# Kernel tuning notes

Measured on AMD Instinct MI355X. Metric: run time of the kernel, lower is better.

## Reference

```python
import jax, jax.numpy as jnp
import numpy as np

B, S, H, SSZ, IN = 1024, 100, 128, 100, 2


def _gru(x, h, Wih, Whh, bih, bhh):
    # PyTorch GRU cell: gates ordered (reset, update, new)
    gx = x @ Wih.T + bih
    gh = h @ Whh.T + bhh
    xr, xz, xn = jnp.split(gx, 3, axis=-1)
    hr, hz, hn = jnp.split(gh, 3, axis=-1)
    r = jax.nn.sigmoid(xr + hr)
    z = jax.nn.sigmoid(xz + hz)
    n = jnp.tanh(xn + r * hn)
    return (1.0 - z) * n + z * h


def _attn(inst_h, rnn_out, W, v):
    # inst_h: [B,S,H], rnn_out: [B,H] -> softmax attention weights [B,S]
    h = jnp.concatenate([inst_h, jnp.broadcast_to(rnn_out[:, None, :], inst_h.shape)], axis=-1)
    s = jax.nn.relu(jnp.einsum('bsk,kh->bsh', h, W)) @ v
    return jax.nn.softmax(s, axis=1)


def setup_inputs() -> dict:
    key = jax.random.key(0)
    k = jax.random.split(key, 32)
    p = lambda i, shape, sc=0.05: sc * jax.random.normal(k[i], shape, jnp.float32)
    instance = jax.random.uniform(k[0], (B, S, IN), jnp.float32)
    # solutions must be per-row permutations of node indices
    solution_1 = jnp.argsort(jax.random.uniform(k[1], (B, S)), axis=1).astype(jnp.int32)
    solution_2 = jnp.argsort(jax.random.uniform(k[2], (B, S)), axis=1).astype(jnp.int32)
    eps = jax.random.normal(k[3], (B, SSZ), jnp.float32)
    return dict(
        instance=instance, solution_1=solution_1, solution_2=solution_2, eps=eps,
        emb_i_W=p(4, (H, IN)), emb_i_b=jnp.zeros(H, jnp.float32),
        emb_r_W=p(5, (H, IN)), emb_r_b=jnp.zeros(H, jnp.float32),
        attn_W=p(6, (2 * H, H)), attn_v=p(7, (H,)),
        gru_Wih=p(8, (3 * H, H)), gru_Whh=p(9, (3 * H, H)),
        gru_bih=jnp.zeros(3 * H, jnp.float32), gru_bhh=jnp.zeros(3 * H, jnp.float32),
        grud_Wih=p(10, (3 * H, 2 * H)), grud_Whh=p(11, (3 * H, H)),
        grud_bih=jnp.zeros(3 * H, jnp.float32), grud_bhh=jnp.zeros(3 * H, jnp.float32),
        enc_fc1_W=p(12, (SSZ, H)), enc_fc1_b=jnp.zeros(SSZ, jnp.float32),
        enc_fc2_W=p(13, (SSZ, H)), enc_fc2_b=jnp.zeros(SSZ, jnp.float32),
        ptr_W=p(14, (2 * H, H)), ptr_v=p(15, (H,)),
        pfc1_W=p(16, (2 * H, 2 * H + SSZ)), pfc1_b=jnp.zeros(2 * H, jnp.float32),
        pfc2_W=p(17, (H, 2 * H)), pfc2_b=jnp.zeros(H, jnp.float32),
    )


def reference(instance, solution_1, solution_2, eps,
              emb_i_W, emb_i_b, emb_r_W, emb_r_b, attn_W, attn_v,
              gru_Wih, gru_Whh, gru_bih, gru_bhh,
              grud_Wih, grud_Whh, grud_bih, grud_bhh,
              enc_fc1_W, enc_fc1_b, enc_fc2_W, enc_fc2_b,
              ptr_W, ptr_v, pfc1_W, pfc1_b, pfc2_W, pfc2_b):
    b_idx = jnp.arange(B)
    inst_h = instance @ emb_i_W.T + emb_i_b  # [B,S,H]
    emb_r = lambda x: x @ emb_r_W.T + emb_r_b
    take = lambda ptr: instance[b_idx, ptr]  # gather node coords [B,IN]

    # ---------------- Encoder ----------------
    def enc_step(carry, ptr):
        h1, h2, ref_h = carry
        h1 = _gru(ref_h, h1, gru_Wih, gru_Whh, gru_bih, gru_bhh)
        a = _attn(inst_h, h1, attn_W, attn_v)
        context = jnp.einsum('bs,bsh->bh', a, inst_h)
        ref_h = emb_r(take(ptr))
        rnn_in = jnp.concatenate([ref_h, context], axis=-1)  # [B,2H]
        h2 = _gru(rnn_in, h2, grud_Wih, grud_Whh, grud_bih, grud_bhh)
        return (h1, h2, ref_h), None

    z0 = jnp.zeros((B, H), instance.dtype)
    ref_h0 = emb_r(take(solution_1[:, 0]))
    (_, h2, _), _ = jax.lax.scan(enc_step, (z0, z0, ref_h0), solution_1[:, 1:].T)
    mu = h2 @ enc_fc1_W.T + enc_fc1_b
    log_var = h2 @ enc_fc2_W.T + enc_fc2_b
    Z = mu + eps * jnp.exp(0.5 * log_var)

    # ---------------- Decoder (teacher forcing) ----------------
    mask0 = jnp.ones((B, S), instance.dtype).at[b_idx, solution_2[:, 0]].set(0.0)

    def dec_step(carry, ptr):
        h1, ref_in, mask = carry
        ref_h = emb_r(ref_in)
        h1 = _gru(ref_h, h1, gru_Wih, gru_Whh, gru_bih, gru_bhh)
        a = _attn(inst_h, h1, attn_W, attn_v)
        context = jnp.einsum('bs,bsh->bh', a, inst_h)
        fc_in = jnp.concatenate([context, Z, ref_h], axis=-1)  # [B, 2H+SSZ]
        fc_out = (fc_in @ pfc1_W.T + pfc1_b) @ pfc2_W.T + pfc2_b  # no activation, as in torch
        hcat = jnp.concatenate([inst_h, jnp.broadcast_to(fc_out[:, None, :], inst_h.shape)], axis=-1)
        logits = jnp.tanh(jnp.einsum('bsk,kh->bsh', hcat, ptr_W)) @ ptr_v  # [B,S]
        probs = jax.nn.softmax(logits + jnp.log(mask), axis=1)
        logp = jnp.log(probs[b_idx, ptr])
        pred = jnp.argmax(probs, axis=1)
        mask = mask.at[b_idx, ptr].set(0.0)  # tsp.update_mask: mark chosen node visited
        return (h1, take(ptr), mask), (pred, logp)

    init = (z0, take(solution_2[:, 0]), mask0)
    _, (preds, logps) = jax.lax.scan(dec_step, init, solution_2[:, 1:].T)
    tour_idx = jnp.concatenate([solution_2[:, :1], preds.T.astype(solution_2.dtype)], axis=1)
    tour_logp = logps.T  # [B, S-1]
    return (mu, log_var, Z, tour_idx, tour_logp)
```

## Files before the change

kernel.cpp:

```cpp
#include <hip/hip_runtime.h>
#include <math.h>

static constexpr int NB  = 1024;
static constexpr int NS  = 100;
static constexpr int NH  = 128;
static constexpr int GPB = 2;
static constexpr int NTHR = 256;
static constexpr int NBLK = NB / GPB;

static constexpr int OUT_MU = 0;
static constexpr int OUT_LV = NB * NS;
static constexpr int OUT_Z  = 2 * NB * NS;
static constexpr int OUT_TI = 3 * NB * NS;
static constexpr int OUT_LP = 4 * NB * NS;

template<int C4>
__device__ __forceinline__ void dot2f(const float* __restrict__ w,
                                      const float* __restrict__ x0, const float* __restrict__ x1,
                                      float& r0, float& r1)
{
    const float4* W = reinterpret_cast<const float4*>(w);
    float a0 = 0.f, a1 = 0.f;
    #pragma unroll 8
    for (int c = 0; c < C4; ++c) {
        float4 u = W[c];
        const float* p0 = x0 + 4 * c;
        const float* p1 = x1 + 4 * c;
        a0 = fmaf(u.x, p0[0], a0); a0 = fmaf(u.y, p0[1], a0);
        a0 = fmaf(u.z, p0[2], a0); a0 = fmaf(u.w, p0[3], a0);
        a1 = fmaf(u.x, p1[0], a1); a1 = fmaf(u.y, p1[1], a1);
        a1 = fmaf(u.z, p1[2], a1); a1 = fmaf(u.w, p1[3], a1);
    }
    r0 = a0; r1 = a1;
}

template<int C4>
__device__ __forceinline__ double dotwd(const float* __restrict__ w, const float* __restrict__ x)
{
    const float4* W = reinterpret_cast<const float4*>(w);
    double a = 0.0;
    #pragma unroll 8
    for (int c = 0; c < C4; ++c) {
        float4 u = W[c];
        const float* p = x + 4 * c;
        a = fma((double)u.x, (double)p[0], a);
        a = fma((double)u.y, (double)p[1], a);
        a = fma((double)u.z, (double)p[2], a);
        a = fma((double)u.w, (double)p[3], a);
    }
    return a;
}

template<int C4>
__device__ __forceinline__ float dot1f(const float* __restrict__ w, const float* __restrict__ x)
{
    const float4* W = reinterpret_cast<const float4*>(w);
    float a = 0.f;
    #pragma unroll 8
    for (int c = 0; c < C4; ++c) {
        float4 u = W[c];
        const float* p = x + 4 * c;
        a = fmaf(u.x, p[0], a); a = fmaf(u.y, p[1], a);
        a = fmaf(u.z, p[2], a); a = fmaf(u.w, p[3], a);
    }
    return a;
}

__device__ __forceinline__ void gru_combine(const float* __restrict__ bih, const float* __restrict__ bhh,
        const float* __restrict__ pa, const float* __restrict__ pb, float* __restrict__ h, int j)
{
    double r = 1.0 / (1.0 + exp(-(((double)pa[j]        + (double)bih[j])        + ((double)pb[j]        + (double)bhh[j]))));
    double z = 1.0 / (1.0 + exp(-(((double)pa[NH + j]   + (double)bih[NH + j])   + ((double)pb[NH + j]   + (double)bhh[NH + j]))));
    double n = tanh(((double)pa[2*NH + j] + (double)bih[2*NH + j]) + r * ((double)pb[2*NH + j] + (double)bhh[2*NH + j]));
    h[j] = (float)((1.0 - z) * n + z * (double)h[j]);
}

__global__ __launch_bounds__(NTHR) void vae_v9(
    const float* __restrict__ instance, const int* __restrict__ sol1,
    const int* __restrict__ sol2, const float* __restrict__ eps,
    const float* __restrict__ emb_i_W, const float* __restrict__ emb_i_b,
    const float* __restrict__ emb_r_W, const float* __restrict__ emb_r_b,
    const float* __restrict__ attn_W, const float* __restrict__ attn_v,
    const float* __restrict__ gru_Wih, const float* __restrict__ gru_Whh,
    const float* __restrict__ gru_bih, const float* __restrict__ gru_bhh,
    const float* __restrict__ grud_Wih, const float* __restrict__ grud_Whh,
    const float* __restrict__ grud_bih, const float* __restrict__ grud_bhh,
    const float* __restrict__ efc1_W, const float* __restrict__ efc1_b,
    const float* __restrict__ efc2_W, const float* __restrict__ efc2_b,
    const float* __restrict__ ptr_W, const float* __restrict__ ptr_v,
    const float* __restrict__ pfc1_W, const float* __restrict__ pfc1_b,
    const float* __restrict__ pfc2_W, const float* __restrict__ pfc2_b,
    float* __restrict__ out)
{
    __shared__ float  s_x[GPB][360];
    __shared__ float  s_h1[GPB][NH], s_h2[GPB][NH], s_fco[GPB][NH];
    __shared__ float  s_fch[GPB][256];
    __shared__ float  s_pa[GPB][3 * NH], s_pb[GPB][3 * NH];
    __shared__ double s_qh[GPB][NH];
    __shared__ double dA0a[NH], dA1a[NH], dAba[NH];
    __shared__ double dA0p[NH], dA1p[NH], dAbp[NH];
    __shared__ float  s_lg[GPB][NS], s_a[GPB][NS];
    __shared__ float  s_c0[GPB][NS], s_c1[GPB][NS], s_msk[GPB][NS];
    __shared__ float  t_wi0[NH], t_wi1[NH], t_bi[NH];
    __shared__ float  t_wr0[NH], t_wr1[NH], t_br[NH];
    __shared__ float  t_va[NH], t_vp[NH];
    __shared__ float  s_rc0[GPB], s_rc1[GPB];
    __shared__ double s_mx[GPB], s_se[GPB];

    const int tid = threadIdx.x;
    const int bbase = blockIdx.x * GPB;
    const int j = tid & (NH - 1);
    const int half = tid >> 7;

    if (tid < NH) {
        t_wi0[tid] = emb_i_W[2*tid]; t_wi1[tid] = emb_i_W[2*tid+1]; t_bi[tid] = emb_i_b[tid];
        t_wr0[tid] = emb_r_W[2*tid]; t_wr1[tid] = emb_r_W[2*tid+1]; t_br[tid] = emb_r_b[tid];
        t_va[tid] = attn_v[tid]; t_vp[tid] = ptr_v[tid];
    }
    for (int i = tid; i < GPB * NS; i += NTHR) {
        int g = i / NS, s = i - g * NS;
        s_c0[g][s] = instance[(size_t)((bbase + g) * NS + s) * 2 + 0];
        s_c1[g][s] = instance[(size_t)((bbase + g) * NS + s) * 2 + 1];
    }
    s_h1[half][j] = 0.f;
    s_h2[half][j] = 0.f;
    __syncthreads();
    {
        const float* Wm = (half == 0) ? attn_W : ptr_W;
        double a0 = 0.0, a1 = 0.0, ab = 0.0;
        for (int k = 0; k < NH; ++k) {
            double wv = (double)Wm[(size_t)k * NH + j];
            a0 = fma((double)t_wi0[k], wv, a0);
            a1 = fma((double)t_wi1[k], wv, a1);
            ab = fma((double)t_bi[k],  wv, ab);
        }
        if (half == 0) { dA0a[j] = a0; dA1a[j] = a1; dAba[j] = ab; }
        else           { dA0p[j] = a0; dA1p[j] = a1; dAbp[j] = ab; }
    }
    {
        int sp = sol1[(bbase + half) * NS + 0];
        s_x[half][j] = fmaf(s_c0[half][sp], t_wr0[j], fmaf(s_c1[half][sp], t_wr1[j], t_br[j]));
    }
    __syncthreads();

    for (int t = 1; t < NS; ++t) {
        if (half == 0) {
            float r0, r1;
            dot2f<32>(gru_Wih + (size_t)j          * NH, s_x[0], s_x[1], r0, r1); s_pa[0][j] = r0;        s_pa[1][j] = r1;
            dot2f<32>(gru_Wih + (size_t)(NH + j)   * NH, s_x[0], s_x[1], r0, r1); s_pa[0][NH + j] = r0;   s_pa[1][NH + j] = r1;
            dot2f<32>(gru_Wih + (size_t)(2*NH + j) * NH, s_x[0], s_x[1], r0, r1); s_pa[0][2*NH + j] = r0; s_pa[1][2*NH + j] = r1;
        } else {
            float r0, r1;
            dot2f<32>(gru_Whh + (size_t)j          * NH, s_h1[0], s_h1[1], r0, r1); s_pb[0][j] = r0;        s_pb[1][j] = r1;
            dot2f<32>(gru_Whh + (size_t)(NH + j)   * NH, s_h1[0], s_h1[1], r0, r1); s_pb[0][NH + j] = r0;   s_pb[1][NH + j] = r1;
            dot2f<32>(gru_Whh + (size_t)(2*NH + j) * NH, s_h1[0], s_h1[1], r0, r1); s_pb[0][2*NH + j] = r0; s_pb[1][2*NH + j] = r1;
        }
        __syncthreads();
        gru_combine(gru_bih, gru_bhh, s_pa[half], s_pb[half], s_h1[half], j);
        __syncthreads();
        {
            const float* col = attn_W + (size_t)NH * NH + j;
            double a = 0.0;
            for (int k = 0; k < NH; ++k) a = fma((double)col[(size_t)k * NH], (double)s_h1[half][k], a);
            s_qh[half][j] = dAba[j] + a;
        }
        __syncthreads();
        if (j < NS) {
            double c0s = (double)s_c0[half][j], c1s = (double)s_c1[half][j];
            double acc = 0.0;
            for (int h = 0; h < NH; ++h) {
                double pre = fma(c0s, dA0a[h], fma(c1s, dA1a[h], s_qh[half][h]));
                acc = fma(fmax(pre, 0.0), (double)t_va[h], acc);
            }
            s_lg[half][j] = (float)acc;
        }
        __syncthreads();
        if (tid < GPB) {
            double mx = -1e308;
            for (int s = 0; s < NS; ++s) if ((double)s_lg[tid][s] > mx) mx = (double)s_lg[tid][s];
            s_mx[tid] = mx;
        }
        __syncthreads();
        if (j < NS) s_a[half][j] = (float)exp((double)s_lg[half][j] - s_mx[half]);
        __syncthreads();
        if (tid < GPB) {
            double se = 0.0;
            for (int s = 0; s < NS; ++s) se += (double)s_a[tid][s];
            s_se[tid] = se;
        }
        __syncthreads();
        if (j < NS) s_a[half][j] = (float)((double)s_a[half][j] / s_se[half]);
        __syncthreads();
        {
            double a = 0.0;
            for (int s = 0; s < NS; ++s) {
                float ih = fmaf(s_c0[half][s], t_wi0[j], fmaf(s_c1[half][s], t_wi1[j], t_bi[j]));
                a += (double)s_a[half][s] * (double)ih;
            }
            int sp = sol1[(bbase + half) * NS + t];
            s_x[half][NH + j] = (float)a;
            s_x[half][j] = fmaf(s_c0[half][sp], t_wr0[j], fmaf(s_c1[half][sp], t_wr1[j], t_br[j]));
        }
        __syncthreads();
        if (half == 0) {
            float r0, r1;
            dot2f<64>(grud_Wih + (size_t)j          * 256, s_x[0], s_x[1], r0, r1); s_pa[0][j] = r0;        s_pa[1][j] = r1;
            dot2f<64>(grud_Wih + (size_t)(NH + j)   * 256, s_x[0], s_x[1], r0, r1); s_pa[0][NH + j] = r0;   s_pa[1][NH + j] = r1;
            dot2f<64>(grud_Wih + (size_t)(2*NH + j) * 256, s_x[0], s_x[1], r0, r1); s_pa[0][2*NH + j] = r0; s_pa[1][2*NH + j] = r1;
        } else {
            float r0, r1;
            dot2f<32>(grud_Whh + (size_t)j          * NH, s_h2[0], s_h2[1], r0, r1); s_pb[0][j] = r0;        s_pb[1][j] = r1;
            dot2f<32>(grud_Whh + (size_t)(NH + j)   * NH, s_h2[0], s_h2[1], r0, r1); s_pb[0][NH + j] = r0;   s_pb[1][NH + j] = r1;
            dot2f<32>(grud_Whh + (size_t)(2*NH + j) * NH, s_h2[0], s_h2[1], r0, r1); s_pb[0][2*NH + j] = r0; s_pb[1][2*NH + j] = r1;
        }
        __syncthreads();
        gru_combine(grud_bih, grud_bhh, s_pa[half], s_pb[half], s_h2[half], j);
        __syncthreads();
    }

    if (j < NS) {
        int s = j, b = bbase + half;
        double mu = dotwd<32>(efc1_W + (size_t)s * NH, s_h2[half]) + (double)efc1_b[s];
        double lv = dotwd<32>(efc2_W + (size_t)s * NH, s_h2[half]) + (double)efc2_b[s];
        double z  = mu + (double)eps[(size_t)b * NS + s] * exp(0.5 * lv);
        out[OUT_MU + b * NS + s] = (float)mu;
        out[OUT_LV + b * NS + s] = (float)lv;
        out[OUT_Z  + b * NS + s] = (float)z;
        s_x[half][NH + s] = (float)z;
    }
    for (int i = tid; i < GPB * NS; i += NTHR) {
        int g = i / NS, s = i - g * NS;
        s_msk[g][s] = 1.f;
    }
    s_h1[half][j] = 0.f;
    __syncthreads();
    if (tid < GPB) {
        int b = bbase + tid;
        int s0 = sol2[b * NS + 0];
        s_msk[tid][s0] = 0.f;
        s_rc0[tid] = s_c0[tid][s0];
        s_rc1[tid] = s_c1[tid][s0];
        out[OUT_TI + b * NS + 0] = (float)s0;
    }
    __syncthreads();

    for (int t = 1; t < NS; ++t) {
        s_x[half][228 + j] = fmaf(s_rc0[half], t_wr0[j], fmaf(s_rc1[half], t_wr1[j], t_br[j]));
        __syncthreads();
        if (half == 0) {
            float r0, r1;
            dot2f<32>(gru_Wih + (size_t)j          * NH, s_x[0] + 228, s_x[1] + 228, r0, r1); s_pa[0][j] = r0;        s_pa[1][j] = r1;
            dot2f<32>(gru_Wih + (size_t)(NH + j)   * NH, s_x[0] + 228, s_x[1] + 228, r0, r1); s_pa[0][NH + j] = r0;   s_pa[1][NH + j] = r1;
            dot2f<32>(gru_Wih + (size_t)(2*NH + j) * NH, s_x[0] + 228, s_x[1] + 228, r0, r1); s_pa[0][2*NH + j] = r0; s_pa[1][2*NH + j] = r1;
        } else {
            float r0, r1;
            dot2f<32>(gru_Whh + (size_t)j          * NH, s_h1[0], s_h1[1], r0, r1); s_pb[0][j] = r0;        s_pb[1][j] = r1;
            dot2f<32>(gru_Whh + (size_t)(NH + j)   * NH, s_h1[0], s_h1[1], r0, r1); s_pb[0][NH + j] = r0;   s_pb[1][NH + j] = r1;
            dot2f<32>(gru_Whh + (size_t)(2*NH + j) * NH, s_h1[0], s_h1[1], r0, r1); s_pb[0][2*NH + j] = r0; s_pb[1][2*NH + j] = r1;
        }
        __syncthreads();
        gru_combine(gru_bih, gru_bhh, s_pa[half], s_pb[half], s_h1[half], j);
        __syncthreads();
        {
            const float* col = attn_W + (size_t)NH * NH + j;
            double a = 0.0;
            for (int k = 0; k < NH; ++k) a = fma((double)col[(size_t)k * NH], (double)s_h1[half][k], a);
            s_qh[half][j] = dAba[j] + a;
        }
        __syncthreads();
        if (j < NS) {
            double c0s = (double)s_c0[half][j], c1s = (double)s_c1[half][j];
            double acc = 0.0;
            for (int h = 0; h < NH; ++h) {
                double pre = fma(c0s, dA0a[h], fma(c1s, dA1a[h], s_qh[half][h]));
                acc = fma(fmax(pre, 0.0), (double)t_va[h], acc);
            }
            s_lg[half][j] = (float)acc;
        }
        __syncthreads();
        if (tid < GPB) {
            double mx = -1e308;
            for (int s = 0; s < NS; ++s) if ((double)s_lg[tid][s] > mx) mx = (double)s_lg[tid][s];
            s_mx[tid] = mx;
        }
        __syncthreads();
        if (j < NS) s_a[half][j] = (float)exp((double)s_lg[half][j] - s_mx[half]);
        __syncthreads();
        if (tid < GPB) {
            double se = 0.0;
            for (int s = 0; s < NS; ++s) se += (double)s_a[tid][s];
            s_se[tid] = se;
        }
        __syncthreads();
        if (j < NS) s_a[half][j] = (float)((double)s_a[half][j] / s_se[half]);
        __syncthreads();
        {
            double a = 0.0;
            for (int s = 0; s < NS; ++s) {
                float ih = fmaf(s_c0[half][s], t_wi0[j], fmaf(s_c1[half][s], t_wi1[j], t_bi[j]));
                a += (double)s_a[half][s] * (double)ih;
            }
            s_x[half][j] = (float)a;
        }
        __syncthreads();
        {
            float r0, r1;
            dot2f<89>(pfc1_W + (size_t)tid * 356, s_x[0], s_x[1], r0, r1);
            float bb = pfc1_b[tid];
            s_fch[0][tid] = r0 + bb;
            s_fch[1][tid] = r1 + bb;
        }
        __syncthreads();
        s_fco[half][j] = dot1f<64>(pfc2_W + (size_t)j * 256, s_fch[half]) + pfc2_b[j];
        __syncthreads();
        {
            const float* col = ptr_W + (size_t)NH * NH + j;
            double a = 0.0;
            for (int k = 0; k < NH; ++k) a = fma((double)col[(size_t)k * NH], (double)s_fco[half][k], a);
            s_qh[half][j] = dAbp[j] + a;
        }
        __syncthreads();
        if (j < NS) {
            double c0s = (double)s_c0[half][j], c1s = (double)s_c1[half][j];
            double acc = 0.0;
            for (int h = 0; h < NH; ++h) {
                double pre = fma(c0s, dA0p[h], fma(c1s, dA1p[h], s_qh[half][h]));
                acc = fma((double)tanhf((float)pre), (double)t_vp[h], acc);
            }
            s_lg[half][j] = (float)acc;
        }
        __syncthreads();
        if (tid < GPB) {
            double mx = -1e308;
            for (int s = 0; s < NS; ++s) {
                double v = (s_msk[tid][s] > 0.f) ? (double)s_lg[tid][s] : -1e308;
                if (v > mx) mx = v;
            }
            s_mx[tid] = mx;
        }
        __syncthreads();
        if (j < NS)
            s_a[half][j] = (s_msk[half][j] > 0.f) ? (float)exp((double)s_lg[half][j] - s_mx[half]) : 0.f;
        __syncthreads();
        if (tid < GPB) {
            int b = bbase + tid;
            int pt = sol2[b * NS + t];
            double se = 0.0;
            for (int s = 0; s < NS; ++s) se += (double)s_a[tid][s];
            double bp = -1.0; int bidx = 0;
            for (int s = 0; s < NS; ++s) {
                double p = (double)s_a[tid][s] / se;
                if (p > bp) { bp = p; bidx = s; }
            }
            double logp = log(((double)s_a[tid][pt]) / se);
            out[OUT_TI + b * NS + t]             = (float)bidx;
            out[OUT_LP + b * (NS - 1) + (t - 1)] = (float)logp;
            s_msk[tid][pt] = 0.f;
            s_rc0[tid] = s_c0[tid][pt];
            s_rc1[tid] = s_c1[tid][pt];
        }
        __syncthreads();
    }
}

extern "C" void kernel_launch(void* const* d_in, const int* in_sizes, int n_in,
                              void* d_out, int out_size, void* d_ws, size_t ws_size,
                              hipStream_t stream)
{
    (void)in_sizes; (void)n_in; (void)out_size; (void)d_ws; (void)ws_size;
    vae_v9<<<NBLK, NTHR, 0, stream>>>(
        (const float*)d_in[0], (const int*)d_in[1], (const int*)d_in[2], (const float*)d_in[3],
        (const float*)d_in[4], (const float*)d_in[5], (const float*)d_in[6], (const float*)d_in[7],
        (const float*)d_in[8], (const float*)d_in[9], (const float*)d_in[10], (const float*)d_in[11],
        (const float*)d_in[12], (const float*)d_in[13], (const float*)d_in[14], (const float*)d_in[15],
        (const float*)d_in[16], (const float*)d_in[17], (const float*)d_in[18], (const float*)d_in[19],
        (const float*)d_in[20], (const float*)d_in[21], (const float*)d_in[22], (const float*)d_in[23],
        (const float*)d_in[24], (const float*)d_in[25], (const float*)d_in[26], (const float*)d_in[27],
        (float*)d_out);
}
```

Measured before the change: 14.27 ms.

## Process four batch rows per block and parallelize softmax reductions

Doubles the batch rows per block from two to four, so each weight row loaded for the GRU and FC matvecs is reused across four inputs (new dot4f helper), and each thread now handles two rows in the per-element phases. Serial single-thread max/sum/argmax loops over the sequence are replaced with 16-lane partial reductions followed by a short final reduction. The grid halves to 256 blocks, which may leave many of the GPU's compute units idle, and shared memory and register use grow per block.

```diff
diff --git a/kernel.cpp b/kernel.cpp
--- a/kernel.cpp
+++ b/kernel.cpp
@@ -4,7 +4,7 @@
 static constexpr int NB  = 1024;
 static constexpr int NS  = 100;
 static constexpr int NH  = 128;
-static constexpr int GPB = 2;
+static constexpr int GPB = 4;
 static constexpr int NTHR = 256;
 static constexpr int NBLK = NB / GPB;
 
@@ -14,22 +14,40 @@
 static constexpr int OUT_TI = 3 * NB * NS;
 static constexpr int OUT_LP = 4 * NB * NS;
 
+#define NEGF (-3.4e38f)
+
+template<int C4>
+__device__ __forceinline__ void dot4f(const float* __restrict__ w,
+        const float* __restrict__ x0, const float* __restrict__ x1,
+        const float* __restrict__ x2, const float* __restrict__ x3,
+        float& r0, float& r1, float& r2, float& r3)
+{
+    const float4* W = reinterpret_cast<const float4*>(w);
+    float a0 = 0.f, a1 = 0.f, a2 = 0.f, a3 = 0.f;
+    #pragma unroll 4
+    for (int c = 0; c < C4; ++c) {
+        float4 u = W[c];
+        int k = 4 * c;
+        a0 = fmaf(u.x, x0[k], a0); a0 = fmaf(u.y, x0[k+1], a0); a0 = fmaf(u.z, x0[k+2], a0); a0 = fmaf(u.w, x0[k+3], a0);
+        a1 = fmaf(u.x, x1[k], a1); a1 = fmaf(u.y, x1[k+1], a1); a1 = fmaf(u.z, x1[k+2], a1); a1 = fmaf(u.w, x1[k+3], a1);
+        a2 = fmaf(u.x, x2[k], a2); a2 = fmaf(u.y, x2[k+1], a2); a2 = fmaf(u.z, x2[k+2], a2); a2 = fmaf(u.w, x2[k+3], a2);
+        a3 = fmaf(u.x, x3[k], a3); a3 = fmaf(u.y, x3[k+1], a3); a3 = fmaf(u.z, x3[k+2], a3); a3 = fmaf(u.w, x3[k+3], a3);
+    }
+    r0 = a0; r1 = a1; r2 = a2; r3 = a3;
+}
+
 template<int C4>
 __device__ __forceinline__ void dot2f(const float* __restrict__ w,
-                                      const float* __restrict__ x0, const float* __restrict__ x1,
-                                      float& r0, float& r1)
+        const float* __restrict__ x0, const float* __restrict__ x1, float& r0, float& r1)
 {
     const float4* W = reinterpret_cast<const float4*>(w);
     float a0 = 0.f, a1 = 0.f;
     #pragma unroll 8
     for (int c = 0; c < C4; ++c) {
         float4 u = W[c];
-        const float* p0 = x0 + 4 * c;
-        const float* p1 = x1 + 4 * c;
-        a0 = fmaf(u.x, p0[0], a0); a0 = fmaf(u.y, p0[1], a0);
-        a0 = fmaf(u.z, p0[2], a0); a0 = fmaf(u.w, p0[3], a0);
-        a1 = fmaf(u.x, p1[0], a1); a1 = fmaf(u.y, p1[1], a1);
-        a1 = fmaf(u.z, p1[2], a1); a1 = fmaf(u.w, p1[3], a1);
+        int k = 4 * c;
+        a0 = fmaf(u.x, x0[k], a0); a0 = fmaf(u.y, x0[k+1], a0); a0 = fmaf(u.z, x0[k+2], a0); a0 = fmaf(u.w, x0[k+3], a0);
+        a1 = fmaf(u.x, x1[k], a1); a1 = fmaf(u.y, x1[k+1], a1); a1 = fmaf(u.z, x1[k+2], a1); a1 = fmaf(u.w, x1[k+3], a1);
     }
     r0 = a0; r1 = a1;
 }
@@ -51,22 +69,7 @@
     return a;
 }
 
-template<int C4>
-__device__ __forceinline__ float dot1f(const float* __restrict__ w, const float* __restrict__ x)
-{
-    const float4* W = reinterpret_cast<const float4*>(w);
-    float a = 0.f;
-    #pragma unroll 8
-    for (int c = 0; c < C4; ++c) {
-        float4 u = W[c];
-        const float* p = x + 4 * c;
-        a = fmaf(u.x, p[0], a); a = fmaf(u.y, p[1], a);
-        a = fmaf(u.z, p[2], a); a = fmaf(u.w, p[3], a);
-    }
-    return a;
-}
-
-__device__ __forceinline__ void gru_combine(const float* __restrict__ bih, const float* __restrict__ bhh,
+__device__ __forceinline__ void gruc(const float* __restrict__ bih, const float* __restrict__ bhh,
         const float* __restrict__ pa, const float* __restrict__ pb, float* __restrict__ h, int j)
 {
     double r = 1.0 / (1.0 + exp(-(((double)pa[j]        + (double)bih[j])        + ((double)pb[j]        + (double)bhh[j]))));
@@ -75,7 +78,7 @@
     h[j] = (float)((1.0 - z) * n + z * (double)h[j]);
 }
 
-__global__ __launch_bounds__(NTHR) void vae_v9(
+__global__ __launch_bounds__(NTHR) void vae_v11(
     const float* __restrict__ instance, const int* __restrict__ sol1,
     const int* __restrict__ sol2, const float* __restrict__ eps,
     const float* __restrict__ emb_i_W, const float* __restrict__ emb_i_b,
@@ -104,13 +107,19 @@
     __shared__ float  t_wi0[NH], t_wi1[NH], t_bi[NH];
     __shared__ float  t_wr0[NH], t_wr1[NH], t_br[NH];
     __shared__ float  t_va[NH], t_vp[NH];
+    __shared__ float  s_red[GPB][16];
+    __shared__ double s_redd[GPB][16];
+    __shared__ int    s_ri[GPB][16];
+    __shared__ float  s_mx[GPB];
+    __shared__ double s_se[GPB];
+    __shared__ int    s_aid[GPB];
     __shared__ float  s_rc0[GPB], s_rc1[GPB];
-    __shared__ double s_mx[GPB], s_se[GPB];
 
     const int tid = threadIdx.x;
     const int bbase = blockIdx.x * GPB;
     const int j = tid & (NH - 1);
     const int half = tid >> 7;
+    const int g0 = half, g1 = half + 2;
 
     if (tid < NH) {
         t_wi0[tid] = emb_i_W[2*tid]; t_wi1[tid] = emb_i_W[2*tid+1]; t_bi[tid] = emb_i_b[tid];
@@ -122,8 +131,8 @@
         s_c0[g][s] = instance[(size_t)((bbase + g) * NS + s) * 2 + 0];
         s_c1[g][s] = instance[(size_t)((bbase + g) * NS + s) * 2 + 1];
     }
-    s_h1[half][j] = 0.f;
-    s_h2[half][j] = 0.f;
+    s_h1[g0][j] = 0.f; s_h1[g1][j] = 0.f;
+    s_h2[g0][j] = 0.f; s_h2[g1][j] = 0.f;
     __syncthreads();
     {
         const float* Wm = (half == 0) ? attn_W : ptr_W;
@@ -138,101 +147,151 @@
         else           { dA0p[j] = a0; dA1p[j] = a1; dAbp[j] = ab; }
     }
     {
-        int sp = sol1[(bbase + half) * NS + 0];
-        s_x[half][j] = fmaf(s_c0[half][sp], t_wr0[j], fmaf(s_c1[half][sp], t_wr1[j], t_br[j]));
+        int sp0 = sol1[(bbase + g0) * NS + 0];
+        int sp1 = sol1[(bbase + g1) * NS + 0];
+        s_x[g0][j] = fmaf(s_c0[g0][sp0], t_wr0[j], fmaf(s_c1[g0][sp0], t_wr1[j], t_br[j]));
+        s_x[g1][j] = fmaf(s_c0[g1][sp1], t_wr0[j], fmaf(s_c1[g1][sp1], t_wr1[j], t_br[j]));
     }
     __syncthreads();
 
     for (int t = 1; t < NS; ++t) {
         if (half == 0) {
-            float r0, r1;
-            dot2f<32>(gru_Wih + (size_t)j          * NH, s_x[0], s_x[1], r0, r1); s_pa[0][j] = r0;        s_pa[1][j] = r1;
-            dot2f<32>(gru_Wih + (size_t)(NH + j)   * NH, s_x[0], s_x[1], r0, r1); s_pa[0][NH + j] = r0;   s_pa[1][NH + j] = r1;
-            dot2f<32>(gru_Wih + (size_t)(2*NH + j) * NH, s_x[0], s_x[1], r0, r1); s_pa[0][2*NH + j] = r0; s_pa[1][2*NH + j] = r1;
+            float r0, r1, r2, r3;
+            dot4f<32>(gru_Wih + (size_t)j          * NH, s_x[0], s_x[1], s_x[2], s_x[3], r0, r1, r2, r3);
+            s_pa[0][j] = r0; s_pa[1][j] = r1; s_pa[2][j] = r2; s_pa[3][j] = r3;
+            dot4f<32>(gru_Wih + (size_t)(NH + j)   * NH, s_x[0], s_x[1], s_x[2], s_x[3], r0, r1, r2, r3);
+            s_pa[0][NH + j] = r0; s_pa[1][NH + j] = r1; s_pa[2][NH + j] = r2; s_pa[3][NH + j] = r3;
+            dot4f<32>(gru_Wih + (size_t)(2*NH + j) * NH, s_x[0], s_x[1], s_x[2], s_x[3], r0, r1, r2, r3);
+            s_pa[0][2*NH + j] = r0; s_pa[1][2*NH + j] = r1; s_pa[2][2*NH + j] = r2; s_pa[3][2*NH + j] = r3;
         } else {
-            float r0, r1;
-            dot2f<32>(gru_Whh + (size_t)j          * NH, s_h1[0], s_h1[1], r0, r1); s_pb[0][j] = r0;        s_pb[1][j] = r1;
-            dot2f<32>(gru_Whh + (size_t)(NH + j)   * NH, s_h1[0], s_h1[1], r0, r1); s_pb[0][NH + j] = r0;   s_pb[1][NH + j] = r1;
-            dot2f<32>(gru_Whh + (size_t)(2*NH + j) * NH, s_h1[0], s_h1[1], r0, r1); s_pb[0][2*NH + j] = r0; s_pb[1][2*NH + j] = r1;
-        }
-        __syncthreads();
-        gru_combine(gru_bih, gru_bhh, s_pa[half], s_pb[half], s_h1[half], j);
+            float r0, r1, r2, r3;
+            dot4f<32>(gru_Whh + (size_t)j          * NH, s_h1[0], s_h1[1], s_h1[2], s_h1[3], r0, r1, r2, r3);
+            s_pb[0][j] = r0; s_pb[1][j] = r1; s_pb[2][j] = r2; s_pb[3][j] = r3;
+            dot4f<32>(gru_Whh + (size_t)(NH + j)   * NH, s_h1[0], s_h1[1], s_h1[2], s_h1[3], r0, r1, r2, r3);
+            s_pb[0][NH + j] = r0; s_pb[1][NH + j] = r1; s_pb[2][NH + j] = r2; s_pb[3][NH + j] = r3;
+            dot4f<32>(gru_Whh + (size_t)(2*NH + j) * NH, s_h1[0], s_h1[1], s_h1[2], s_h1[3], r0, r1, r2, r3);
+            s_pb[0][2*NH + j] = r0; s_pb[1][2*NH + j] = r1; s_pb[2][2*NH + j] = r2; s_pb[3][2*NH + j] = r3;
+        }
+        __syncthreads();
+        gruc(gru_bih, gru_bhh, s_pa[g0], s_pb[g0], s_h1[g0], j);
+        gruc(gru_bih, gru_bhh, s_pa[g1], s_pb[g1], s_h1[g1], j);
         __syncthreads();
         {
             const float* col = attn_W + (size_t)NH * NH + j;
-            double a = 0.0;
-            for (int k = 0; k < NH; ++k) a = fma((double)col[(size_t)k * NH], (double)s_h1[half][k], a);
-            s_qh[half][j] = dAba[j] + a;
-        }
-        __syncthreads();
-        if (j < NS) {
-            double c0s = (double)s_c0[half][j], c1s = (double)s_c1[half][j];
-            double acc = 0.0;
+            double a0 = 0.0, a1 = 0.0;
+            for (int k = 0; k < NH; ++k) {
+                double wv = (double)col[(size_t)k * NH];
+                a0 = fma(wv, (double)s_h1[g0][k], a0);
+                a1 = fma(wv, (double)s_h1[g1][k], a1);
+            }
+            s_qh[g0][j] = dAba[j] + a0;
+            s_qh[g1][j] = dAba[j] + a1;
+        }
+        __syncthreads();
+        if (j < NS) {
+            double c00 = (double)s_c0[g0][j], c10 = (double)s_c1[g0][j];
+            double c01 = (double)s_c0[g1][j], c11 = (double)s_c1[g1][j];
+            double acc0 = 0.0, acc1 = 0.0;
             for (int h = 0; h < NH; ++h) {
-                double pre = fma(c0s, dA0a[h], fma(c1s, dA1a[h], s_qh[half][h]));
-                acc = fma(fmax(pre, 0.0), (double)t_va[h], acc);
-            }
-            s_lg[half][j] = (float)acc;
+                double A0 = dA0a[h], A1 = dA1a[h], v = (double)t_va[h];
+                double p0 = fma(c00, A0, fma(c10, A1, s_qh[g0][h]));
+                double p1 = fma(c01, A0, fma(c11, A1, s_qh[g1][h]));
+                acc0 = fma(fmax(p0, 0.0), v, acc0);
+                acc1 = fma(fmax(p1, 0.0), v, acc1);
+            }
+            s_lg[g0][j] = (float)acc0;
+            s_lg[g1][j] = (float)acc1;
+        }
+        __syncthreads();
+        if (j < 16) {
+            float m0 = NEGF, m1 = NEGF;
+            for (int s = j; s < NS; s += 16) { m0 = fmaxf(m0, s_lg[g0][s]); m1 = fmaxf(m1, s_lg[g1][s]); }
+            s_red[g0][j] = m0; s_red[g1][j] = m1;
         }
         __syncthreads();
         if (tid < GPB) {
-            double mx = -1e308;
-            for (int s = 0; s < NS; ++s) if ((double)s_lg[tid][s] > mx) mx = (double)s_lg[tid][s];
-            s_mx[tid] = mx;
-        }
-        __syncthreads();
-        if (j < NS) s_a[half][j] = (float)exp((double)s_lg[half][j] - s_mx[half]);
+            float m = NEGF;
+            for (int i = 0; i < 16; ++i) m = fmaxf(m, s_red[tid][i]);
+            s_mx[tid] = m;
+        }
+        __syncthreads();
+        if (j < NS) {
+            s_a[g0][j] = (float)exp((double)s_lg[g0][j] - (double)s_mx[g0]);
+            s_a[g1][j] = (float)exp((double)s_lg[g1][j] - (double)s_mx[g1]);
+        }
+        __syncthreads();
+        if (j < 16) {
+            double t0 = 0.0, t1 = 0.0;
+            for (int s = j; s < NS; s += 16) { t0 += (double)s_a[g0][s]; t1 += (double)s_a[g1][s]; }
+            s_redd[g0][j] = t0; s_redd[g1][j] = t1;
+        }
         __syncthreads();
         if (tid < GPB) {
             double se = 0.0;
-            for (int s = 0; s < NS; ++s) se += (double)s_a[tid][s];
+            for (int i = 0; i < 16; ++i) se += s_redd[tid][i];
             s_se[tid] = se;
         }
         __syncthreads();
-        if (j < NS) s_a[half][j] = (float)((double)s_a[half][j] / s_se[half]);
-        __syncthreads();
-        {
-            double a = 0.0;
+        if (j < NS) {
+            s_a[g0][j] = (float)((double)s_a[g0][j] / s_se[g0]);
+            s_a[g1][j] = (float)((double)s_a[g1][j] / s_se[g1]);
+        }
+        __syncthreads();
+        {
+            float w0 = t_wi0[j], w1 = t_wi1[j], bb = t_bi[j];
+            double a0 = 0.0, a1 = 0.0;
             for (int s = 0; s < NS; ++s) {
-                float ih = fmaf(s_c0[half][s], t_wi0[j], fmaf(s_c1[half][s], t_wi1[j], t_bi[j]));
-                a += (double)s_a[half][s] * (double)ih;
-            }
-            int sp = sol1[(bbase + half) * NS + t];
-            s_x[half][NH + j] = (float)a;
-            s_x[half][j] = fmaf(s_c0[half][sp], t_wr0[j], fmaf(s_c1[half][sp], t_wr1[j], t_br[j]));
+                float ih0 = fmaf(s_c0[g0][s], w0, fmaf(s_c1[g0][s], w1, bb));
+                float ih1 = fmaf(s_c0[g1][s], w0, fmaf(s_c1[g1][s], w1, bb));
+                a0 += (double)s_a[g0][s] * (double)ih0;
+                a1 += (double)s_a[g1][s] * (double)ih1;
+            }
+            s_x[g0][NH + j] = (float)a0;
+            s_x[g1][NH + j] = (float)a1;
+            int sp0 = sol1[(bbase + g0) * NS + t];
+            int sp1 = sol1[(bbase + g1) * NS + t];
+            s_x[g0][j] = fmaf(s_c0[g0][sp0], t_wr0[j], fmaf(s_c1[g0][sp0], t_wr1[j], t_br[j]));
+            s_x[g1][j] = fmaf(s_c0[g1][sp1], t_wr0[j], fmaf(s_c1[g1][sp1], t_wr1[j], t_br[j]));
         }
         __syncthreads();
         if (half == 0) {
-            float r0, r1;
-            dot2f<64>(grud_Wih + (size_t)j          * 256, s_x[0], s_x[1], r0, r1); s_pa[0][j] = r0;        s_pa[1][j] = r1;
-            dot2f<64>(grud_Wih + (size_t)(NH + j)   * 256, s_x[0], s_x[1], r0, r1); s_pa[0][NH + j] = r0;   s_pa[1][NH + j] = r1;
-            dot2f<64>(grud_Wih + (size_t)(2*NH + j) * 256, s_x[0], s_x[1], r0, r1); s_pa[0][2*NH + j] = r0; s_pa[1][2*NH + j] = r1;
+            float r0, r1, r2, r3;
+            dot4f<64>(grud_Wih + (size_t)j          * 256, s_x[0], s_x[1], s_x[2], s_x[3], r0, r1, r2, r3);
+            s_pa[0][j] = r0; s_pa[1][j] = r1; s_pa[2][j] = r2; s_pa[3][j] = r3;
+            dot4f<64>(grud_Wih + (size_t)(NH + j)   * 256, s_x[0], s_x[1], s_x[2], s_x[3], r0, r1, r2, r3);
+            s_pa[0][NH + j] = r0; s_pa[1][NH + j] = r1; s_pa[2][NH + j] = r2; s_pa[3][NH + j] = r3;
+            dot4f<64>(grud_Wih + (size_t)(2*NH + j) * 256, s_x[0], s_x[1], s_x[2], s_x[3], r0, r1, r2, r3);
+            s_pa[0][2*NH + j] = r0; s_pa[1][2*NH + j] = r1; s_pa[2][2*NH + j] = r2; s_pa[3][2*NH + j] = r3;
         } else {
-            float r0, r1;
-            dot2f<32>(grud_Whh + (size_t)j          * NH, s_h2[0], s_h2[1], r0, r1); s_pb[0][j] = r0;        s_pb[1][j] = r1;
-            dot2f<32>(grud_Whh + (size_t)(NH + j)   * NH, s_h2[0], s_h2[1], r0, r1); s_pb[0][NH + j] = r0;   s_pb[1][NH + j] = r1;
-            dot2f<32>(grud_Whh + (size_t)(2*NH + j) * NH, s_h2[0], s_h2[1], r0, r1); s_pb[0][2*NH + j] = r0; s_pb[1][2*NH + j] = r1;
-        }
-        __syncthreads();
-        gru_combine(grud_bih, grud_bhh, s_pa[half], s_pb[half], s_h2[half], j);
-        __syncthreads();
-    }
-
-    if (j < NS) {
-        int s = j, b = bbase + half;
-        double mu = dotwd<32>(efc1_W + (size_t)s * NH, s_h2[half]) + (double)efc1_b[s];
-        double lv = dotwd<32>(efc2_W + (size_t)s * NH, s_h2[half]) + (double)efc2_b[s];
+            float r0, r1, r2, r3;
+            dot4f<32>(grud_Whh + (size_t)j          * NH, s_h2[0], s_h2[1], s_h2[2], s_h2[3], r0, r1, r2, r3);
+            s_pb[0][j] = r0; s_pb[1][j] = r1; s_pb[2][j] = r2; s_pb[3][j] = r3;
+            dot4f<32>(grud_Whh + (size_t)(NH + j)   * NH, s_h2[0], s_h2[1], s_h2[2], s_h2[3], r0, r1, r2, r3);
+            s_pb[0][NH + j] = r0; s_pb[1][NH + j] = r1; s_pb[2][NH + j] = r2; s_pb[3][NH + j] = r3;
+            dot4f<32>(grud_Whh + (size_t)(2*NH + j) * NH, s_h2[0], s_h2[1], s_h2[2], s_h2[3], r0, r1, r2, r3);
+            s_pb[0][2*NH + j] = r0; s_pb[1][2*NH + j] = r1; s_pb[2][2*NH + j] = r2; s_pb[3][2*NH + j] = r3;
+        }
+        __syncthreads();
+        gruc(grud_bih, grud_bhh, s_pa[g0], s_pb[g0], s_h2[g0], j);
+        gruc(grud_bih, grud_bhh, s_pa[g1], s_pb[g1], s_h2[g1], j);
+        __syncthreads();
+    }
+
+    for (int idx = tid; idx < GPB * NS; idx += NTHR) {
+        int g = idx / NS, s = idx - g * NS, b = bbase + g;
+        double mu = dotwd<32>(efc1_W + (size_t)s * NH, s_h2[g]) + (double)efc1_b[s];
+        double lv = dotwd<32>(efc2_W + (size_t)s * NH, s_h2[g]) + (double)efc2_b[s];
         double z  = mu + (double)eps[(size_t)b * NS + s] * exp(0.5 * lv);
         out[OUT_MU + b * NS + s] = (float)mu;
         out[OUT_LV + b * NS + s] = (float)lv;
         out[OUT_Z  + b * NS + s] = (float)z;
-        s_x[half][NH + s] = (float)z;
+        s_x[g][NH + s] = (float)z;
     }
     for (int i = tid; i < GPB * NS; i += NTHR) {
         int g = i / NS, s = i - g * NS;
         s_msk[g][s] = 1.f;
     }
-    s_h1[half][j] = 0.f;
+    s_h1[g0][j] = 0.f; s_h1[g1][j] = 0.f;
     __syncthreads();
     if (tid < GPB) {
         int b = bbase + tid;
@@ -245,119 +304,196 @@
     __syncthreads();
 
     for (int t = 1; t < NS; ++t) {
-        s_x[half][228 + j] = fmaf(s_rc0[half], t_wr0[j], fmaf(s_rc1[half], t_wr1[j], t_br[j]));
+        s_x[g0][228 + j] = fmaf(s_rc0[g0], t_wr0[j], fmaf(s_rc1[g0], t_wr1[j], t_br[j]));
+        s_x[g1][228 + j] = fmaf(s_rc0[g1], t_wr0[j], fmaf(s_rc1[g1], t_wr1[j], t_br[j]));
         __syncthreads();
         if (half == 0) {
-            float r0, r1;
-            dot2f<32>(gru_Wih + (size_t)j          * NH, s_x[0] + 228, s_x[1] + 228, r0, r1); s_pa[0][j] = r0;        s_pa[1][j] = r1;
-            dot2f<32>(gru_Wih + (size_t)(NH + j)   * NH, s_x[0] + 228, s_x[1] + 228, r0, r1); s_pa[0][NH + j] = r0;   s_pa[1][NH + j] = r1;
-            dot2f<32>(gru_Wih + (size_t)(2*NH + j) * NH, s_x[0] + 228, s_x[1] + 228, r0, r1); s_pa[0][2*NH + j] = r0; s_pa[1][2*NH + j] = r1;
+            float r0, r1, r2, r3;
+            dot4f<32>(gru_Wih + (size_t)j          * NH, s_x[0]+228, s_x[1]+228, s_x[2]+228, s_x[3]+228, r0, r1, r2, r3);
+            s_pa[0][j] = r0; s_pa[1][j] = r1; s_pa[2][j] = r2; s_pa[3][j] = r3;
+            dot4f<32>(gru_Wih + (size_t)(NH + j)   * NH, s_x[0]+228, s_x[1]+228, s_x[2]+228, s_x[3]+228, r0, r1, r2, r3);
+            s_pa[0][NH + j] = r0; s_pa[1][NH + j] = r1; s_pa[2][NH + j] = r2; s_pa[3][NH + j] = r3;
+            dot4f<32>(gru_Wih + (size_t)(2*NH + j) * NH, s_x[0]+228, s_x[1]+228, s_x[2]+228, s_x[3]+228, r0, r1, r2, r3);
+            s_pa[0][2*NH + j] = r0; s_pa[1][2*NH + j] = r1; s_pa[2][2*NH + j] = r2; s_pa[3][2*NH + j] = r3;
         } else {
-            float r0, r1;
-            dot2f<32>(gru_Whh + (size_t)j          * NH, s_h1[0], s_h1[1], r0, r1); s_pb[0][j] = r0;        s_pb[1][j] = r1;
-            dot2f<32>(gru_Whh + (size_t)(NH + j)   * NH, s_h1[0], s_h1[1], r0, r1); s_pb[0][NH + j] = r0;   s_pb[1][NH + j] = r1;
-            dot2f<32>(gru_Whh + (size_t)(2*NH + j) * NH, s_h1[0], s_h1[1], r0, r1); s_pb[0][2*NH + j] = r0; s_pb[1][2*NH + j] = r1;
-        }
-        __syncthreads();
-        gru_combine(gru_bih, gru_bhh, s_pa[half], s_pb[half], s_h1[half], j);
+            float r0, r1, r2, r3;
+            dot4f<32>(gru_Whh + (size_t)j          * NH, s_h1[0], s_h1[1], s_h1[2], s_h1[3], r0, r1, r2, r3);
+            s_pb[0][j] = r0; s_pb[1][j] = r1; s_pb[2][j] = r2; s_pb[3][j] = r3;
+            dot4f<32>(gru_Whh + (size_t)(NH + j)   * NH, s_h1[0], s_h1[1], s_h1[2], s_h1[3], r0, r1, r2, r3);
+            s_pb[0][NH + j] = r0; s_pb[1][NH + j] = r1; s_pb[2][NH + j] = r2; s_pb[3][NH + j] = r3;
+            dot4f<32>(gru_Whh + (size_t)(2*NH + j) * NH, s_h1[0], s_h1[1], s_h1[2], s_h1[3], r0, r1, r2, r3);
+            s_pb[0][2*NH + j] = r0; s_pb[1][2*NH + j] = r1; s_pb[2][2*NH + j] = r2; s_pb[3][2*NH + j] = r3;
+        }
+        __syncthreads();
+        gruc(gru_bih, gru_bhh, s_pa[g0], s_pb[g0], s_h1[g0], j);
+        gruc(gru_bih, gru_bhh, s_pa[g1], s_pb[g1], s_h1[g1], j);
         __syncthreads();
         {
             const float* col = attn_W + (size_t)NH * NH + j;
-            double a = 0.0;
-            for (int k = 0; k < NH; ++k) a = fma((double)col[(size_t)k * NH], (double)s_h1[half][k], a);
-            s_qh[half][j] = dAba[j] + a;
-        }
-        __syncthreads();
-        if (j < NS) {
-            double c0s = (double)s_c0[half][j], c1s = (double)s_c1[half][j];
-            double acc = 0.0;
+            double a0 = 0.0, a1 = 0.0;
+            for (int k = 0; k < NH; ++k) {
+                double wv = (double)col[(size_t)k * NH];
+                a0 = fma(wv, (double)s_h1[g0][k], a0);
+                a1 = fma(wv, (double)s_h1[g1][k], a1);
+            }
+            s_qh[g0][j] = dAba[j] + a0;
+            s_qh[g1][j] = dAba[j] + a1;
+        }
+        __syncthreads();
+        if (j < NS) {
+            double c00 = (double)s_c0[g0][j], c10 = (double)s_c1[g0][j];
+            double c01 = (double)s_c0[g1][j], c11 = (double)s_c1[g1][j];
+            double acc0 = 0.0, acc1 = 0.0;
             for (int h = 0; h < NH; ++h) {
-                double pre = fma(c0s, dA0a[h], fma(c1s, dA1a[h], s_qh[half][h]));
-                acc = fma(fmax(pre, 0.0), (double)t_va[h], acc);
-            }
-            s_lg[half][j] = (float)acc;
+                double A0 = dA0a[h], A1 = dA1a[h], v = (double)t_va[h];
+                double p0 = fma(c00, A0, fma(c10, A1, s_qh[g0][h]));
+                double p1 = fma(c01, A0, fma(c11, A1, s_qh[g1][h]));
+                acc0 = fma(fmax(p0, 0.0), v, acc0);
+                acc1 = fma(fmax(p1, 0.0), v, acc1);
+            }
+            s_lg[g0][j] = (float)acc0;
+            s_lg[g1][j] = (float)acc1;
+        }
+        __syncthreads();
+        if (j < 16) {
+            float m0 = NEGF, m1 = NEGF;
+            for (int s = j; s < NS; s += 16) { m0 = fmaxf(m0, s_lg[g0][s]); m1 = fmaxf(m1, s_lg[g1][s]); }
+            s_red[g0][j] = m0; s_red[g1][j] = m1;
         }
         __syncthreads();
         if (tid < GPB) {
-            double mx = -1e308;
-            for (int s = 0; s < NS; ++s) if ((double)s_lg[tid][s] > mx) mx = (double)s_lg[tid][s];
-            s_mx[tid] = mx;
-        }
-        __syncthreads();
-        if (j < NS) s_a[half][j] = (float)exp((double)s_lg[half][j] - s_mx[half]);
+            float m = NEGF;
+            for (int i = 0; i < 16; ++i) m = fmaxf(m, s_red[tid][i]);
+            s_mx[tid] = m;
+        }
+        __syncthreads();
+        if (j < NS) {
+            s_a[g0][j] = (float)exp((double)s_lg[g0][j] - (double)s_mx[g0]);
+            s_a[g1][j] = (float)exp((double)s_lg[g1][j] - (double)s_mx[g1]);
+        }
+        __syncthreads();
+        if (j < 16) {
+            double t0 = 0.0, t1 = 0.0;
+            for (int s = j; s < NS; s += 16) { t0 += (double)s_a[g0][s]; t1 += (double)s_a[g1][s]; }
+            s_redd[g0][j] = t0; s_redd[g1][j] = t1;
+        }
         __syncthreads();
         if (tid < GPB) {
             double se = 0.0;
-            for (int s = 0; s < NS; ++s) se += (double)s_a[tid][s];
+            for (int i = 0; i < 16; ++i) se += s_redd[tid][i];
             s_se[tid] = se;
         }
         __syncthreads();
-        if (j < NS) s_a[half][j] = (float)((double)s_a[half][j] / s_se[half]);
-        __syncthreads();
-        {
-            double a = 0.0;
+        if (j < NS) {
+            s_a[g0][j] = (float)((double)s_a[g0][j] / s_se[g0]);
+            s_a[g1][j] = (float)((double)s_a[g1][j] / s_se[g1]);
+        }
+        __syncthreads();
+        {
+            float w0 = t_wi0[j], w1 = t_wi1[j], bb = t_bi[j];
+            double a0 = 0.0, a1 = 0.0;
             for (int s = 0; s < NS; ++s) {
-                float ih = fmaf(s_c0[half][s], t_wi0[j], fmaf(s_c1[half][s], t_wi1[j], t_bi[j]));
-                a += (double)s_a[half][s] * (double)ih;
-            }
-            s_x[half][j] = (float)a;
+                float ih0 = fmaf(s_c0[g0][s], w0, fmaf(s_c1[g0][s], w1, bb));
+                float ih1 = fmaf(s_c0[g1][s], w0, fmaf(s_c1[g1][s], w1, bb));
+                a0 += (double)s_a[g0][s] * (double)ih0;
+                a1 += (double)s_a[g1][s] * (double)ih1;
+            }
+            s_x[g0][j] = (float)a0;
+            s_x[g1][j] = (float)a1;
+        }
+        __syncthreads();
+        {
+            float r0, r1, r2, r3;
+            dot4f<89>(pfc1_W + (size_t)tid * 356, s_x[0], s_x[1], s_x[2], s_x[3], r0, r1, r2, r3);
+            float bb = pfc1_b[tid];
+            s_fch[0][tid] = r0 + bb; s_fch[1][tid] = r1 + bb;
+            s_fch[2][tid] = r2 + bb; s_fch[3][tid] = r3 + bb;
         }
         __syncthreads();
         {
             float r0, r1;
-            dot2f<89>(pfc1_W + (size_t)tid * 356, s_x[0], s_x[1], r0, r1);
-            float bb = pfc1_b[tid];
-            s_fch[0][tid] = r0 + bb;
-            s_fch[1][tid] = r1 + bb;
-        }
-        __syncthreads();
-        s_fco[half][j] = dot1f<64>(pfc2_W + (size_t)j * 256, s_fch[half]) + pfc2_b[j];
+            dot2f<64>(pfc2_W + (size_t)j * 256, s_fch[g0], s_fch[g1], r0, r1);
+            s_fco[g0][j] = r0 + pfc2_b[j];
+            s_fco[g1][j] = r1 + pfc2_b[j];
+        }
         __syncthreads();
         {
             const float* col = ptr_W + (size_t)NH * NH + j;
-            double a = 0.0;
-            for (int k = 0; k < NH; ++k) a = fma((double)col[(size_t)k * NH], (double)s_fco[half][k], a);
-            s_qh[half][j] = dAbp[j] + a;
-        }
-        __syncthreads();
-        if (j < NS) {
-            double c0s = (double)s_c0[half][j], c1s = (double)s_c1[half][j];
-            double acc = 0.0;
+            double a0 = 0.0, a1 = 0.0;
+            for (int k = 0; k < NH; ++k) {
+                double wv = (double)col[(size_t)k * NH];
+                a0 = fma(wv, (double)s_fco[g0][k], a0);
+                a1 = fma(wv, (double)s_fco[g1][k], a1);
+            }
+            s_qh[g0][j] = dAbp[j] + a0;
+            s_qh[g1][j] = dAbp[j] + a1;
+        }
+        __syncthreads();
+        if (j < NS) {
+            double c00 = (double)s_c0[g0][j], c10 = (double)s_c1[g0][j];
+            double c01 = (double)s_c0[g1][j], c11 = (double)s_c1[g1][j];
+            double acc0 = 0.0, acc1 = 0.0;
             for (int h = 0; h < NH; ++h) {
-                double pre = fma(c0s, dA0p[h], fma(c1s, dA1p[h], s_qh[half][h]));
-                acc = fma((double)tanhf((float)pre), (double)t_vp[h], acc);
-            }
-            s_lg[half][j] = (float)acc;
+                double A0 = dA0p[h], A1 = dA1p[h], v = (double)t_vp[h];
+                double p0 = fma(c00, A0, fma(c10, A1, s_qh[g0][h]));
+                double p1 = fma(c01, A0, fma(c11, A1, s_qh[g1][h]));
+                acc0 = fma((double)tanhf((float)p0), v, acc0);
+                acc1 = fma((double)tanhf((float)p1), v, acc1);
+            }
+            s_lg[g0][j] = (float)acc0;
+            s_lg[g1][j] = (float)acc1;
+        }
+        __syncthreads();
+        if (j < 16) {
+            float m0 = NEGF, m1 = NEGF;
+            for (int s = j; s < NS; s += 16) {
+                float v0 = (s_msk[g0][s] > 0.f) ? s_lg[g0][s] : NEGF;
+                float v1 = (s_msk[g1][s] > 0.f) ? s_lg[g1][s] : NEGF;
+                m0 = fmaxf(m0, v0);
+                m1 = fmaxf(m1, v1);
+            }
+            s_red[g0][j] = m0; s_red[g1][j] = m1;
         }
         __syncthreads();
         if (tid < GPB) {
-            double mx = -1e308;
-            for (int s = 0; s < NS; ++s) {
-                double v = (s_msk[tid][s] > 0.f) ? (double)s_lg[tid][s] : -1e308;
-                if (v > mx) mx = v;
-            }
-            s_mx[tid] = mx;
-        }
-        __syncthreads();
-        if (j < NS)
-            s_a[half][j] = (s_msk[half][j] > 0.f) ? (float)exp((double)s_lg[half][j] - s_mx[half]) : 0.f;
+            float m = NEGF;
+            for (int i = 0; i < 16; ++i) m = fmaxf(m, s_red[tid][i]);
+            s_mx[tid] = m;
+        }
+        __syncthreads();
+        if (j < NS) {
+            s_a[g0][j] = (s_msk[g0][j] > 0.f) ? (float)exp((double)s_lg[g0][j] - (double)s_mx[g0]) : 0.f;
+            s_a[g1][j] = (s_msk[g1][j] > 0.f) ? (float)exp((double)s_lg[g1][j] - (double)s_mx[g1]) : 0.f;
+        }
+        __syncthreads();
+        if (j < 16) {
+            float m0 = -1.f, m1 = -1.f; int i0 = 0, i1 = 0;
+            double t0 = 0.0, t1 = 0.0;
+            for (int s = j; s < NS; s += 16) {
+                float a0v = s_a[g0][s], a1v = s_a[g1][s];
+                t0 += (double)a0v; t1 += (double)a1v;
+                if (a0v > m0) { m0 = a0v; i0 = s; }
+                if (a1v > m1) { m1 = a1v; i1 = s; }
+            }
+            s_red[g0][j] = m0; s_ri[g0][j] = i0; s_redd[g0][j] = t0;
+            s_red[g1][j] = m1; s_ri[g1][j] = i1; s_redd[g1][j] = t1;
+        }
         __syncthreads();
         if (tid < GPB) {
-            int b = bbase + tid;
+            int g = tid, b = bbase + g;
+            float m = -1.f; int mi = NS; double se = 0.0;
+            for (int i = 0; i < 16; ++i) {
+                se += s_redd[g][i];
+                float v = s_red[g][i]; int vi = s_ri[g][i];
+                if (v > m || (v == m && vi < mi)) { m = v; mi = vi; }
+            }
             int pt = sol2[b * NS + t];
-            double se = 0.0;
-            for (int s = 0; s < NS; ++s) se += (double)s_a[tid][s];
-            double bp = -1.0; int bidx = 0;
-            for (int s = 0; s < NS; ++s) {
-                double p = (double)s_a[tid][s] / se;
-                if (p > bp) { bp = p; bidx = s; }
-            }
-            double logp = log(((double)s_a[tid][pt]) / se);
-            out[OUT_TI + b * NS + t]             = (float)bidx;
+            double logp = log((double)s_a[g][pt] / se);
+            out[OUT_TI + b * NS + t]             = (float)mi;
             out[OUT_LP + b * (NS - 1) + (t - 1)] = (float)logp;
-            s_msk[tid][pt] = 0.f;
-            s_rc0[tid] = s_c0[tid][pt];
-            s_rc1[tid] = s_c1[tid][pt];
+            s_msk[g][pt] = 0.f;
+            s_rc0[g] = s_c0[g][pt];
+            s_rc1[g] = s_c1[g][pt];
         }
         __syncthreads();
     }
@@ -368,7 +504,7 @@
                               hipStream_t stream)
 {
     (void)in_sizes; (void)n_in; (void)out_size; (void)d_ws; (void)ws_size;
-    vae_v9<<<NBLK, NTHR, 0, stream>>>(
+    vae_v11<<<NBLK, NTHR, 0, stream>>>(
         (const float*)d_in[0], (const int*)d_in[1], (const int*)d_in[2], (const float*)d_in[3],
         (const float*)d_in[4], (const float*)d_in[5], (const float*)d_in[6], (const float*)d_in[7],
         (const float*)d_in[8], (const float*)d_in[9], (const float*)d_in[10], (const float*)d_in[11],
```

New measurement: 14.17 ms. About the same (-0.7%).
